# Optimization experiments

Measured on AMD Instinct MI355X. Metric: run time of the kernel, lower is better.

## Reference

```python
import jax, jax.numpy as jnp
import numpy as np

NUM_GROUPS = 32
RANK = 64            # per-head rank (uniform)
IN_FEATURES = 4096
OUT_FEATURES = 4096
GROUP_DIM = OUT_FEATURES // NUM_GROUPS  # 128
SUM_RANKS = NUM_GROUPS * RANK           # 2048


def setup_inputs() -> dict:
    key = jax.random.key(0)
    k1, k2, k3 = jax.random.split(key, 3)
    hidden_states = jax.random.normal(k1, (4, 4096, IN_FEATURES), dtype=jnp.float32)
    # VT: nn.Linear(in_features, sum(ranks), bias=False) -> weight [sum_ranks, in]
    VT_weight = jax.random.normal(k2, (SUM_RANKS, IN_FEATURES), dtype=jnp.float32) * (1.0 / np.sqrt(IN_FEATURES))
    # U_list: per-group nn.Linear(r, group_dim), init.normal_ -> stacked [G, group_dim, r]
    U_weight = jax.random.normal(k3, (NUM_GROUPS, GROUP_DIM, RANK), dtype=jnp.float32)
    return {"hidden_states": hidden_states, "VT_weight": VT_weight, "U_weight": U_weight}


def reference(hidden_states, VT_weight, U_weight):
    # shared down-projection: [B,S,in] @ [in,sum_ranks] -> [B,S,sum_ranks]
    z = jnp.einsum('bsi,ri->bsr', hidden_states, VT_weight)
    B, S, _ = z.shape
    # grouped up-projection (block-diagonal GEMM): slice per group -> [B,S,G,r]
    zg = z.reshape(B, S, NUM_GROUPS, RANK)
    out = jnp.einsum('bsgr,gdr->bsgd', zg, U_weight)  # [B,S,G,group_dim]
    return out.reshape(B, S, NUM_GROUPS * GROUP_DIM)  # concat along last dim
```

## Files before the change

### kernel.cpp

```cpp
#include <hip/hip_runtime.h>
#include <hip/hip_bf16.h>
#include <stdint.h>

typedef __attribute__((ext_vector_type(8)))  short bf16x8;
typedef __attribute__((ext_vector_type(4)))  float f32x4;
typedef __attribute__((ext_vector_type(4)))  float float4v;
typedef __attribute__((ext_vector_type(8)))  unsigned short u16x8;

#define MFMA16(a,b,c) __builtin_amdgcn_mfma_f32_16x16x32_bf16((a),(b),(c),0,0,0)

__device__ __forceinline__ unsigned short f2bf(float f) {
    unsigned int u = __builtin_bit_cast(unsigned int, f);
    u = (u + 0x7fffu + ((u >> 16) & 1u)) >> 16;
    return (unsigned short)u;
}

__device__ __forceinline__ void gload_lds16(const void* g, void* l) {
    __builtin_amdgcn_global_load_lds(
        (const __attribute__((address_space(1))) void*)g,
        (__attribute__((address_space(3))) void*)l, 16, 0, 0);
}

template<int N> __device__ __forceinline__ void waitvm() {}
template<> __device__ __forceinline__ void waitvm<6>() { asm volatile("s_waitcnt vmcnt(6)" ::: "memory"); }
template<> __device__ __forceinline__ void waitvm<4>() { asm volatile("s_waitcnt vmcnt(4)" ::: "memory"); }
template<> __device__ __forceinline__ void waitvm<2>() { asm volatile("s_waitcnt vmcnt(2)" ::: "memory"); }
template<> __device__ __forceinline__ void waitvm<0>() { asm volatile("s_waitcnt vmcnt(0)" ::: "memory"); }

__global__ void cvt_f32_bf16(const float* __restrict__ in, unsigned short* __restrict__ out, long n) {
    long i = ((long)blockIdx.x * blockDim.x + threadIdx.x) * 8;
    long stride = (long)gridDim.x * blockDim.x * 8;
    for (; i < n; i += stride) {
        float4v v0 = *(const float4v*)(in + i);
        float4v v1 = *(const float4v*)(in + i + 4);
        u16x8 o;
        o[0] = f2bf(v0[0]); o[1] = f2bf(v0[1]); o[2] = f2bf(v0[2]); o[3] = f2bf(v0[3]);
        o[4] = f2bf(v1[0]); o[5] = f2bf(v1[1]); o[6] = f2bf(v1[2]); o[7] = f2bf(v1[3]);
        *(u16x8*)(out + i) = o;
    }
}


#define STAGE_A(nA_, k0n, h, l) \
    gload_lds16(pA + ((l)*128 + (h)*64) * 4096L + (k0n), (nA_) + dA0 + ((l)*128 + (h)*64) * 64)
#define STAGE_B(nB_, k0n, h, l) \
    gload_lds16(pB + ((l)*128 + (h)*32) * 4096L + (k0n), (nB_) + dB0 + ((l)*128 + (h)*32) * 64)

#define LDA(sA_, QM) do { _Pragma("unroll") for (int mi = 0; mi < 4; ++mi) { \
    a[mi][0] = *(const bf16x8*)((sA_) + ((wr*128 + (QM)*64 + mi*16 + lan15) << 6) + g0); \
    a[mi][1] = *(const bf16x8*)((sA_) + ((wr*128 + (QM)*64 + mi*16 + lan15) << 6) + (g0 ^ 32)); } } while (0)
#define LDB(sB_, QN) do { _Pragma("unroll") for (int ni = 0; ni < 2; ++ni) { \
    b[ni][0] = *(const bf16x8*)((sB_) + ((wc*64 + (QN)*32 + ni*16 + lan15) << 6) + g0); \
    b[ni][1] = *(const bf16x8*)((sB_) + ((wc*64 + (QN)*32 + ni*16 + lan15) << 6) + (g0 ^ 32)); } } while (0)

#define DOMFMA(QM, QN) do { __builtin_amdgcn_s_setprio(1); \
    _Pragma("unroll") for (int mi = 0; mi < 4; ++mi) \
      _Pragma("unroll") for (int ni = 0; ni < 2; ++ni) { \
        acc[(QM)*4+mi][(QN)*2+ni] = MFMA16(a[mi][0], b[ni][0], acc[(QM)*4+mi][(QN)*2+ni]); \
        acc[(QM)*4+mi][(QN)*2+ni] = MFMA16(a[mi][1], b[ni][1], acc[(QM)*4+mi][(QN)*2+ni]); } \
    __builtin_amdgcn_s_setprio(0); } while (0)

#define BAR1() do { __builtin_amdgcn_s_barrier(); \
    asm volatile("s_waitcnt lgkmcnt(0)" ::: "memory"); \
    __builtin_amdgcn_sched_barrier(0); } while (0)
#define BAR2() do { __builtin_amdgcn_s_barrier(); \
    __builtin_amdgcn_sched_barrier(0); } while (0)

#define KTILE(sA_, sB_, nA_, nB_, k0n, DOSTAGE, V0, V1, V3) do { \
     \
    LDA(sA_, 0); LDB(sB_, 0); \
    if (DOSTAGE) { STAGE_A(nA_, k0n, 0, 0); STAGE_A(nA_, k0n, 0, 1); \
                   STAGE_B(nB_, k0n, 0, 0); STAGE_B(nB_, k0n, 0, 1); } \
    BAR1(); DOMFMA(0, 0); waitvm<V0>(); BAR2(); \
     \
    LDB(sB_, 1); \
    if (DOSTAGE) { STAGE_B(nB_, k0n, 1, 0); STAGE_B(nB_, k0n, 1, 1); } \
    BAR1(); DOMFMA(0, 1); waitvm<V1>(); BAR2(); \
     \
    LDA(sA_, 1); \
    if (DOSTAGE) { STAGE_A(nA_, k0n, 1, 0); STAGE_A(nA_, k0n, 1, 1); } \
    BAR1(); DOMFMA(1, 1); BAR2(); \
     \
    LDB(sB_, 0); \
    BAR1(); DOMFMA(1, 0); waitvm<V3>(); BAR2(); \
} while (0)

__global__ __launch_bounds__(512, 2) void gemm1_8ph(const unsigned short* __restrict__ A,
                                                    const unsigned short* __restrict__ B,
                                                    unsigned short* __restrict__ Z) {
    __shared__ __align__(16) unsigned short lds[65536];

    const int tid   = threadIdx.x;
    const int lane  = tid & 63;
    const int wid   = tid >> 6;
    const int wr    = wid >> 2;
    const int wc    = wid & 3;
    const int lan15 = lane & 15;
    const int g0    = (((lane >> 4) ^ (lane & 7)) << 3);

    const int  bid = blockIdx.x;
    const long m0  = (long)(bid >> 3) * 256;
    const long n0  = (long)(bid & 7) * 256;

    const int q     = tid >> 3;
    const int granA = (((tid & 7) ^ (q & 7)) << 3);
    const unsigned short* pA = A + (m0 + q) * 4096L + granA;
    const int rB0   = (q & 31) + ((q >> 5) << 6);
    const unsigned short* pB = B + (n0 + rB0) * 4096L + granA;
    const int dA0   = (wid * 8) * 64;
    const int dB0   = ((wid & 3) * 8 + ((wid >> 2) << 6)) * 64;

    f32x4 acc[8][4] = {};
    bf16x8 a[4][2], b[2][2];

    unsigned short* buf0 = lds;
    unsigned short* buf1 = lds + 32768;

    STAGE_A(buf0, 0, 0, 0); STAGE_A(buf0, 0, 0, 1);
    STAGE_B(buf0 + 16384, 0, 0, 0); STAGE_B(buf0 + 16384, 0, 0, 1);
    STAGE_B(buf0 + 16384, 0, 1, 0); STAGE_B(buf0 + 16384, 0, 1, 1);
    STAGE_A(buf0, 0, 1, 0); STAGE_A(buf0, 0, 1, 1);
    waitvm<4>();
    BAR2();

    for (int t = 0; t < 63; ++t) {
        unsigned short* cb = (t & 1) ? buf1 : buf0;
        unsigned short* nb = (t & 1) ? buf0 : buf1;
        KTILE(cb, cb + 16384, nb, nb + 16384, (t + 1) * 64, true, 6, 6, 4);
    }
    KTILE(buf1, buf1 + 16384, buf0, buf0 + 16384, 0, false, 2, 0, -1);

    const int rq = (lane >> 4) << 2;
    #pragma unroll
    for (int mi = 0; mi < 8; ++mi) {
        #pragma unroll
        for (int ni = 0; ni < 4; ++ni) {
            const long mb = m0 + wr * 128 + mi * 16 + rq;
            const long nb2 = n0 + wc * 64 + ni * 16 + lan15;
            #pragma unroll
            for (int j = 0; j < 4; ++j)
                Z[(mb + j) * 2048L + nb2] = f2bf(acc[mi][ni][j]);
        }
    }
}

#define U_PAD 80

__global__ __launch_bounds__(256) void gemm2(const unsigned short* __restrict__ Z,
                                             const float* __restrict__ U,
                                             float* __restrict__ out) {
    __shared__ __align__(16) unsigned short lU[128 * U_PAD];

    const int tid  = threadIdx.x;
    const int lane = tid & 63;
    const int wid  = tid >> 6;
    const int g    = blockIdx.x & 31;
    const long m0  = (long)(blockIdx.x >> 5) * 64;

    const float* ug = U + (long)g * (128 * 64);
    for (int i = tid; i < (128 * 64) / 4; i += 256) {
        const int r = i >> 4;
        const int c = (i << 2) & 63;
        float4v v = *(const float4v*)(ug + i * 4);
        unsigned short* d = &lU[r * U_PAD + c];
        d[0] = f2bf(v[0]); d[1] = f2bf(v[1]); d[2] = f2bf(v[2]); d[3] = f2bf(v[3]);
    }
    __syncthreads();

    const long mrow = m0 + wid * 16 + (lane & 15);
    const unsigned short* zrow = Z + mrow * 2048L + g * 64 + ((lane >> 4) << 3);
    const bf16x8 a0 = *(const bf16x8*)(zrow);
    const bf16x8 a1 = *(const bf16x8*)(zrow + 32);

    f32x4 acc[8] = {};
    const int blds = (lane & 15);
    const int kofs = (lane >> 4) << 3;
    #pragma unroll
    for (int ni = 0; ni < 8; ++ni) {
        const bf16x8 b0 = *(const bf16x8*)&lU[(ni * 16 + blds) * U_PAD + kofs];
        const bf16x8 b1 = *(const bf16x8*)&lU[(ni * 16 + blds) * U_PAD + 32 + kofs];
        acc[ni] = MFMA16(a0, b0, acc[ni]);
        acc[ni] = MFMA16(a1, b1, acc[ni]);
    }

    const long mb = m0 + wid * 16 + ((lane >> 4) << 2);
    const long cb = (long)g * 128 + (lane & 15);
    #pragma unroll
    for (int ni = 0; ni < 8; ++ni)
        #pragma unroll
        for (int j = 0; j < 4; ++j)
            out[(mb + j) * 4096L + cb + ni * 16] = acc[ni][j];
}

extern "C" void kernel_launch(void* const* d_in, const int* in_sizes, int n_in,
                              void* d_out, int out_size, void* d_ws, size_t ws_size,
                              hipStream_t stream) {
    const float* hs = (const float*)d_in[0];
    const float* vt = (const float*)d_in[1];
    const float* uw = (const float*)d_in[2];
    float* out = (float*)d_out;

    unsigned short* hs_bf = (unsigned short*)d_ws;
    unsigned short* vt_bf = hs_bf + 67108864L;
    unsigned short* z_bf  = vt_bf + 8388608L;

    cvt_f32_bf16<<<2048, 256, 0, stream>>>(hs, hs_bf, 67108864L);
    cvt_f32_bf16<<<512, 256, 0, stream>>>(vt, vt_bf, 8388608L);

    gemm1_8ph<<<512, 512, 0, stream>>>(hs_bf, vt_bf, z_bf);

    gemm2<<<8192, 256, 0, stream>>>(z_bf, uw, out);
}
```

Baseline: 377.0 us.

## Fuse grouped up-projection into down-projection GEMM epilogue via LDS

Removes the separate gemm2 kernel and the Z intermediate in global memory. Each wave stages its bf16 Z tile into swizzled LDS after the main loop, loads its group's U weights into registers (converted to bf16), and runs the block-diagonal up-projection MFMAs directly, writing fp32 output with vector stores. This avoids the round trip of the Z tensor through HBM and one kernel launch, at the cost of more register pressure and a longer epilogue in the main GEMM.

```diff
diff --git a/kernel.cpp b/kernel.cpp
--- a/kernel.cpp
+++ b/kernel.cpp
@@ -67,27 +67,24 @@
     __builtin_amdgcn_sched_barrier(0); } while (0)
 
 #define KTILE(sA_, sB_, nA_, nB_, k0n, DOSTAGE, V0, V1, V3) do { \
-     \
     LDA(sA_, 0); LDB(sB_, 0); \
     if (DOSTAGE) { STAGE_A(nA_, k0n, 0, 0); STAGE_A(nA_, k0n, 0, 1); \
                    STAGE_B(nB_, k0n, 0, 0); STAGE_B(nB_, k0n, 0, 1); } \
     BAR1(); DOMFMA(0, 0); waitvm<V0>(); BAR2(); \
-     \
     LDB(sB_, 1); \
     if (DOSTAGE) { STAGE_B(nB_, k0n, 1, 0); STAGE_B(nB_, k0n, 1, 1); } \
     BAR1(); DOMFMA(0, 1); waitvm<V1>(); BAR2(); \
-     \
     LDA(sA_, 1); \
     if (DOSTAGE) { STAGE_A(nA_, k0n, 1, 0); STAGE_A(nA_, k0n, 1, 1); } \
     BAR1(); DOMFMA(1, 1); BAR2(); \
-     \
     LDB(sB_, 0); \
     BAR1(); DOMFMA(1, 0); waitvm<V3>(); BAR2(); \
 } while (0)
 
-__global__ __launch_bounds__(512, 2) void gemm1_8ph(const unsigned short* __restrict__ A,
-                                                    const unsigned short* __restrict__ B,
-                                                    unsigned short* __restrict__ Z) {
+__global__ __launch_bounds__(512, 2) void gemm_fused(const unsigned short* __restrict__ A,
+                                                     const unsigned short* __restrict__ B,
+                                                     const float* __restrict__ Uw,
+                                                     float* __restrict__ out) {
     __shared__ __align__(16) unsigned short lds[65536];
 
     const int tid   = threadIdx.x;
@@ -102,10 +99,10 @@
     const long m0  = (long)(bid >> 3) * 256;
     const long n0  = (long)(bid & 7) * 256;
 
-    const int q     = tid >> 3;
-    const int granA = (((tid & 7) ^ (q & 7)) << 3);
-    const unsigned short* pA = A + (m0 + q) * 4096L + granA;
-    const int rB0   = (q & 31) + ((q >> 5) << 6);
+    const int q8    = tid >> 3;
+    const int granA = (((tid & 7) ^ (q8 & 7)) << 3);
+    const unsigned short* pA = A + (m0 + q8) * 4096L + granA;
+    const int rB0   = (q8 & 31) + ((q8 >> 5) << 6);
     const unsigned short* pB = B + (n0 + rB0) * 4096L + granA;
     const int dA0   = (wid * 8) * 64;
     const int dB0   = ((wid & 3) * 8 + ((wid >> 2) << 6)) * 64;
@@ -130,66 +127,59 @@
     }
     KTILE(buf1, buf1 + 16384, buf0, buf0 + 16384, 0, false, 2, 0, -1);
 
-    const int rq = (lane >> 4) << 2;
-    #pragma unroll
-    for (int mi = 0; mi < 8; ++mi) {
+    {
+        unsigned short* zw = lds + wid * 8192;
+        const int q = lane >> 4;
+
         #pragma unroll
-        for (int ni = 0; ni < 4; ++ni) {
-            const long mb = m0 + wr * 128 + mi * 16 + rq;
-            const long nb2 = n0 + wc * 64 + ni * 16 + lan15;
-            #pragma unroll
-            for (int j = 0; j < 4; ++j)
-                Z[(mb + j) * 2048L + nb2] = f2bf(acc[mi][ni][j]);
+        for (int mi = 0; mi < 8; ++mi) {
+            #pragma unroll
+            for (int ni = 0; ni < 4; ++ni) {
+                #pragma unroll
+                for (int j = 0; j < 4; ++j) {
+                    const int ml = mi * 16 + q * 4 + j;
+                    const int gr = (ni * 2 + (lan15 >> 3)) ^ (ml & 7);
+                    zw[ml * 64 + gr * 8 + (lan15 & 7)] = f2bf(acc[mi][ni][j]);
+                }
+            }
+        }
+
+        const int g_blk = (bid & 7) * 4 + wc;
+        const float* ug = Uw + (long)g_blk * 8192;
+        bf16x8 ua[2][8];
+        #pragma unroll
+        for (int df = 0; df < 8; ++df) {
+            #pragma unroll
+            for (int rk = 0; rk < 2; ++rk) {
+                const float* up = ug + (df * 16 + lan15) * 64 + rk * 32 + q * 8;
+                float4v u0 = *(const float4v*)up;
+                float4v u1 = *(const float4v*)(up + 4);
+                u16x8 t;
+                t[0] = f2bf(u0[0]); t[1] = f2bf(u0[1]); t[2] = f2bf(u0[2]); t[3] = f2bf(u0[3]);
+                t[4] = f2bf(u1[0]); t[5] = f2bf(u1[1]); t[6] = f2bf(u1[2]); t[7] = f2bf(u1[3]);
+                ua[rk][df] = __builtin_bit_cast(bf16x8, t);
+            }
+        }
+
+        const long mwb  = m0 + wr * 128;
+        const long ocol = (long)g_blk * 128;
+        #pragma unroll
+        for (int mf = 0; mf < 8; ++mf) {
+            f32x4 a2[8] = {};
+            #pragma unroll
+            for (int rk = 0; rk < 2; ++rk) {
+                const int ml = mf * 16 + lan15;
+                const int gr = (rk * 4 + q) ^ (ml & 7);
+                const bf16x8 zb = *(const bf16x8*)&zw[ml * 64 + gr * 8];
+                #pragma unroll
+                for (int df = 0; df < 8; ++df)
+                    a2[df] = MFMA16(ua[rk][df], zb, a2[df]);
+            }
+            #pragma unroll
+            for (int df = 0; df < 8; ++df)
+                *(float4v*)&out[(mwb + mf * 16 + lan15) * 4096L + ocol + df * 16 + q * 4] = a2[df];
         }
     }
-}
-
-#define U_PAD 80
-
-__global__ __launch_bounds__(256) void gemm2(const unsigned short* __restrict__ Z,
-                                             const float* __restrict__ U,
-                                             float* __restrict__ out) {
-    __shared__ __align__(16) unsigned short lU[128 * U_PAD];
-
-    const int tid  = threadIdx.x;
-    const int lane = tid & 63;
-    const int wid  = tid >> 6;
-    const int g    = blockIdx.x & 31;
-    const long m0  = (long)(blockIdx.x >> 5) * 64;
-
-    const float* ug = U + (long)g * (128 * 64);
-    for (int i = tid; i < (128 * 64) / 4; i += 256) {
-        const int r = i >> 4;
-        const int c = (i << 2) & 63;
-        float4v v = *(const float4v*)(ug + i * 4);
-        unsigned short* d = &lU[r * U_PAD + c];
-        d[0] = f2bf(v[0]); d[1] = f2bf(v[1]); d[2] = f2bf(v[2]); d[3] = f2bf(v[3]);
-    }
-    __syncthreads();
-
-    const long mrow = m0 + wid * 16 + (lane & 15);
-    const unsigned short* zrow = Z + mrow * 2048L + g * 64 + ((lane >> 4) << 3);
-    const bf16x8 a0 = *(const bf16x8*)(zrow);
-    const bf16x8 a1 = *(const bf16x8*)(zrow + 32);
-
-    f32x4 acc[8] = {};
-    const int blds = (lane & 15);
-    const int kofs = (lane >> 4) << 3;
-    #pragma unroll
-    for (int ni = 0; ni < 8; ++ni) {
-        const bf16x8 b0 = *(const bf16x8*)&lU[(ni * 16 + blds) * U_PAD + kofs];
-        const bf16x8 b1 = *(const bf16x8*)&lU[(ni * 16 + blds) * U_PAD + 32 + kofs];
-        acc[ni] = MFMA16(a0, b0, acc[ni]);
-        acc[ni] = MFMA16(a1, b1, acc[ni]);
-    }
-
-    const long mb = m0 + wid * 16 + ((lane >> 4) << 2);
-    const long cb = (long)g * 128 + (lane & 15);
-    #pragma unroll
-    for (int ni = 0; ni < 8; ++ni)
-        #pragma unroll
-        for (int j = 0; j < 4; ++j)
-            out[(mb + j) * 4096L + cb + ni * 16] = acc[ni][j];
 }
 
 extern "C" void kernel_launch(void* const* d_in, const int* in_sizes, int n_in,
@@ -202,12 +192,9 @@
 
     unsigned short* hs_bf = (unsigned short*)d_ws;
     unsigned short* vt_bf = hs_bf + 67108864L;
-    unsigned short* z_bf  = vt_bf + 8388608L;
 
     cvt_f32_bf16<<<2048, 256, 0, stream>>>(hs, hs_bf, 67108864L);
     cvt_f32_bf16<<<512, 256, 0, stream>>>(vt, vt_bf, 8388608L);
 
-    gemm1_8ph<<<512, 512, 0, stream>>>(hs_bf, vt_bf, z_bf);
-
-    gemm2<<<8192, 256, 0, stream>>>(z_bf, uw, out);
-}
+    gemm_fused<<<512, 512, 0, stream>>>(hs_bf, vt_bf, uw, out);
+}
```

New measurement: 389.7 us. 3.4% more time.

## Fuse fp32-to-bf16 conversion of activations into GEMM1 A-tile loading

Applied to the files above, without the earlier changes.

Removes the separate conversion kernel for hidden_states and instead has GEMM1 load fp32 A tiles into registers, convert them to bf16 and write them swizzled into LDS, with register double-buffering (arE/arO) one tile ahead. This avoids writing and re-reading a 128MB bf16 copy of the activations, at the cost of higher register pressure, register-to-LDS stores in place of direct global-to-LDS loads, and a reworked vmcnt wait schedule. GEMM1 now reads fp32 A, which doubles its A-side global traffic, but the extra pass over the activations is gone.

```diff
diff --git a/kernel.cpp b/kernel.cpp
--- a/kernel.cpp
+++ b/kernel.cpp
@@ -6,6 +6,7 @@
 typedef __attribute__((ext_vector_type(4)))  float f32x4;
 typedef __attribute__((ext_vector_type(4)))  float float4v;
 typedef __attribute__((ext_vector_type(8)))  unsigned short u16x8;
+typedef __attribute__((ext_vector_type(4)))  unsigned short u16x4;
 
 #define MFMA16(a,b,c) __builtin_amdgcn_mfma_f32_16x16x32_bf16((a),(b),(c),0,0,0)
 
@@ -22,10 +23,10 @@
 }
 
 template<int N> __device__ __forceinline__ void waitvm() {}
-template<> __device__ __forceinline__ void waitvm<6>() { asm volatile("s_waitcnt vmcnt(6)" ::: "memory"); }
-template<> __device__ __forceinline__ void waitvm<4>() { asm volatile("s_waitcnt vmcnt(4)" ::: "memory"); }
-template<> __device__ __forceinline__ void waitvm<2>() { asm volatile("s_waitcnt vmcnt(2)" ::: "memory"); }
-template<> __device__ __forceinline__ void waitvm<0>() { asm volatile("s_waitcnt vmcnt(0)" ::: "memory"); }
+template<> __device__ __forceinline__ void waitvm<0>()  { asm volatile("s_waitcnt vmcnt(0)"  ::: "memory"); }
+template<> __device__ __forceinline__ void waitvm<8>()  { asm volatile("s_waitcnt vmcnt(8)"  ::: "memory"); }
+template<> __device__ __forceinline__ void waitvm<10>() { asm volatile("s_waitcnt vmcnt(10)" ::: "memory"); }
+template<> __device__ __forceinline__ void waitvm<12>() { asm volatile("s_waitcnt vmcnt(12)" ::: "memory"); }
 
 __global__ void cvt_f32_bf16(const float* __restrict__ in, unsigned short* __restrict__ out, long n) {
     long i = ((long)blockIdx.x * blockDim.x + threadIdx.x) * 8;
@@ -41,8 +42,6 @@
 }
 
 
-#define STAGE_A(nA_, k0n, h, l) \
-    gload_lds16(pA + ((l)*128 + (h)*64) * 4096L + (k0n), (nA_) + dA0 + ((l)*128 + (h)*64) * 64)
 #define STAGE_B(nB_, k0n, h, l) \
     gload_lds16(pB + ((l)*128 + (h)*32) * 4096L + (k0n), (nB_) + dB0 + ((l)*128 + (h)*32) * 64)
 
@@ -66,26 +65,32 @@
 #define BAR2() do { __builtin_amdgcn_s_barrier(); \
     __builtin_amdgcn_sched_barrier(0); } while (0)
 
-#define KTILE(sA_, sB_, nA_, nB_, k0n, DOSTAGE, V0, V1, V3) do { \
-     \
-    LDA(sA_, 0); LDB(sB_, 0); \
-    if (DOSTAGE) { STAGE_A(nA_, k0n, 0, 0); STAGE_A(nA_, k0n, 0, 1); \
-                   STAGE_B(nB_, k0n, 0, 0); STAGE_B(nB_, k0n, 0, 1); } \
+#define ALOAD(ar_, kA) do { _Pragma("unroll") for (int ii = 0; ii < 8; ++ii) \
+    ar_[ii] = *(const float4v*)(pAf + (long)ii * 16384 + (kA)); } while (0)
+
+#define ACVT(dst_, ar_) do { _Pragma("unroll") for (int ii = 0; ii < 8; ++ii) { \
+    u16x4 pk; pk[0] = f2bf(ar_[ii][0]); pk[1] = f2bf(ar_[ii][1]); \
+              pk[2] = f2bf(ar_[ii][2]); pk[3] = f2bf(ar_[ii][3]); \
+    const int rl = rbase + ii * 4; \
+    *(u16x4*)((dst_) + rl * 64 + ((gA ^ (rl & 7)) << 3) + hA) = pk; } } while (0)
+
+#define KTILE2(cbA_, cbB_, nbA_, nbB_, kB, kA, arI_, arC_, DOSTAGE, V0, V3) do { \
+    LDA(cbA_, 0); LDB(cbB_, 0); \
+    if (DOSTAGE) { STAGE_B(nbB_, kB, 0, 0); STAGE_B(nbB_, kB, 0, 1); \
+                   __builtin_amdgcn_sched_barrier(0); \
+                   ALOAD(arI_, kA); } \
     BAR1(); DOMFMA(0, 0); waitvm<V0>(); BAR2(); \
-     \
-    LDB(sB_, 1); \
-    if (DOSTAGE) { STAGE_B(nB_, k0n, 1, 0); STAGE_B(nB_, k0n, 1, 1); } \
-    BAR1(); DOMFMA(0, 1); waitvm<V1>(); BAR2(); \
-     \
-    LDA(sA_, 1); \
-    if (DOSTAGE) { STAGE_A(nA_, k0n, 1, 0); STAGE_A(nA_, k0n, 1, 1); } \
+    LDB(cbB_, 1); \
+    if (DOSTAGE) { STAGE_B(nbB_, kB, 1, 0); STAGE_B(nbB_, kB, 1, 1); } \
+    BAR1(); DOMFMA(0, 1); BAR2(); \
+    LDA(cbA_, 1); \
     BAR1(); DOMFMA(1, 1); BAR2(); \
-     \
-    LDB(sB_, 0); \
+    LDB(cbB_, 0); \
+    if (DOSTAGE) { ACVT(nbA_, arC_); } \
     BAR1(); DOMFMA(1, 0); waitvm<V3>(); BAR2(); \
 } while (0)
 
-__global__ __launch_bounds__(512, 2) void gemm1_8ph(const unsigned short* __restrict__ A,
+__global__ __launch_bounds__(512, 2) void gemm1_8ph(const float* __restrict__ Af,
                                                     const unsigned short* __restrict__ B,
                                                     unsigned short* __restrict__ Z) {
     __shared__ __align__(16) unsigned short lds[65536];
@@ -102,40 +107,54 @@
     const long m0  = (long)(bid >> 3) * 256;
     const long n0  = (long)(bid & 7) * 256;
 
-    const int q     = tid >> 3;
-    const int granA = (((tid & 7) ^ (q & 7)) << 3);
-    const unsigned short* pA = A + (m0 + q) * 4096L + granA;
-    const int rB0   = (q & 31) + ((q >> 5) << 6);
+    const int q8    = tid >> 3;
+    const int granA = (((tid & 7) ^ (q8 & 7)) << 3);
+    const int rB0   = (q8 & 31) + ((q8 >> 5) << 6);
     const unsigned short* pB = B + (n0 + rB0) * 4096L + granA;
-    const int dA0   = (wid * 8) * 64;
     const int dB0   = ((wid & 3) * 8 + ((wid >> 2) << 6)) * 64;
+
+    const int rbase = wid * 32 + (lane >> 4);
+    const float* pAf = Af + (m0 + rbase) * 4096L + (lan15 & 15) * 4;
+    const int gA = lan15 >> 1;
+    const int hA = (lane & 1) * 4;
 
     f32x4 acc[8][4] = {};
     bf16x8 a[4][2], b[2][2];
+    float4v arE[8], arO[8];
 
     unsigned short* buf0 = lds;
     unsigned short* buf1 = lds + 32768;
 
-    STAGE_A(buf0, 0, 0, 0); STAGE_A(buf0, 0, 0, 1);
+    ALOAD(arE, 0);
     STAGE_B(buf0 + 16384, 0, 0, 0); STAGE_B(buf0 + 16384, 0, 0, 1);
     STAGE_B(buf0 + 16384, 0, 1, 0); STAGE_B(buf0 + 16384, 0, 1, 1);
-    STAGE_A(buf0, 0, 1, 0); STAGE_A(buf0, 0, 1, 1);
-    waitvm<4>();
-    BAR2();
-
-    for (int t = 0; t < 63; ++t) {
-        unsigned short* cb = (t & 1) ? buf1 : buf0;
-        unsigned short* nb = (t & 1) ? buf0 : buf1;
-        KTILE(cb, cb + 16384, nb, nb + 16384, (t + 1) * 64, true, 6, 6, 4);
-    }
-    KTILE(buf1, buf1 + 16384, buf0, buf0 + 16384, 0, false, 2, 0, -1);
+    __builtin_amdgcn_sched_barrier(0);
+    ALOAD(arO, 64);
+    waitvm<12>();
+    ACVT(buf0, arE);
+    waitvm<8>();
+    asm volatile("s_waitcnt lgkmcnt(0)" ::: "memory");
+    __builtin_amdgcn_s_barrier();
+    __builtin_amdgcn_sched_barrier(0);
+
+    for (int it = 0; it < 31; ++it) {
+        const int t = it * 2;
+        KTILE2(buf0, buf0 + 16384, buf1, buf1 + 16384,
+               (t + 1) * 64, (t + 2) * 64, arE, arO, true, 10, 10);
+        KTILE2(buf1, buf1 + 16384, buf0, buf0 + 16384,
+               (t + 2) * 64, (t + 3) * 64, arO, arE, true, 10, 10);
+    }
+    KTILE2(buf0, buf0 + 16384, buf1, buf1 + 16384,
+           63 * 64, 63 * 64, arE, arO, true, 10, 10);
+    KTILE2(buf1, buf1 + 16384, buf0, buf0 + 16384,
+           0, 0, arE, arO, false, 0, -1);
 
     const int rq = (lane >> 4) << 2;
     #pragma unroll
     for (int mi = 0; mi < 8; ++mi) {
         #pragma unroll
         for (int ni = 0; ni < 4; ++ni) {
-            const long mb = m0 + wr * 128 + mi * 16 + rq;
+            const long mb  = m0 + wr * 128 + mi * 16 + rq;
             const long nb2 = n0 + wc * 64 + ni * 16 + lan15;
             #pragma unroll
             for (int j = 0; j < 4; ++j)
@@ -200,14 +219,12 @@
     const float* uw = (const float*)d_in[2];
     float* out = (float*)d_out;
 
-    unsigned short* hs_bf = (unsigned short*)d_ws;
-    unsigned short* vt_bf = hs_bf + 67108864L;
+    unsigned short* vt_bf = (unsigned short*)d_ws;
     unsigned short* z_bf  = vt_bf + 8388608L;
 
-    cvt_f32_bf16<<<2048, 256, 0, stream>>>(hs, hs_bf, 67108864L);
     cvt_f32_bf16<<<512, 256, 0, stream>>>(vt, vt_bf, 8388608L);
 
-    gemm1_8ph<<<512, 512, 0, stream>>>(hs_bf, vt_bf, z_bf);
+    gemm1_8ph<<<512, 512, 0, stream>>>(hs, vt_bf, z_bf);
 
     gemm2<<<8192, 256, 0, stream>>>(z_bf, uw, out);
 }
```

Result: slower. 963.2 us (+155.5%).
